# Kernel tuning notes

Measured on AMD Instinct MI355X. Metric: run time of the kernel, lower is better.

The kernel has to match this reference:

```python
import jax, jax.numpy as jnp
import numpy as np

BS, T, NOBJ = 16, 32, 100
GLOVE, GEMB, ADIM, GCN_DIM, H, ASPACE, RES = 300, 64, 10, 512, 512, 6, 512


def setup_inputs() -> dict:
    key = jax.random.key(0)
    ks = jax.random.split(key, 34)
    rn = lambda k, shp, s=0.02: (jax.random.normal(k, shp, jnp.float32) * s)
    inp = {}
    inp["target"] = jax.random.normal(ks[0], (BS, T, GLOVE), jnp.float32)
    inp["input_"] = jax.random.normal(ks[1], (BS, T, RES, 1, 1), jnp.float32)
    inp["action_probs"] = jax.random.uniform(ks[2], (BS, T, ASPACE), jnp.float32)
    # symmetric normalized adjacency (D^-1/2 A D^-1/2), as normalize_adj produces
    A_raw = (jax.random.uniform(ks[3], (NOBJ, NOBJ)) < 0.1).astype(jnp.float32)
    A_raw = ((A_raw + A_raw.T + jnp.eye(NOBJ)) > 0).astype(jnp.float32)
    dinv = 1.0 / jnp.sqrt(jnp.sum(A_raw, axis=1))
    inp["A"] = A_raw * dinv[:, None] * dinv[None, :]
    inp["all_glove"] = jax.random.normal(ks[4], (NOBJ, GLOVE), jnp.float32)
    inp["Wword"] = rn(ks[5], (GEMB, GLOVE)); inp["bword"] = jnp.zeros((GEMB,))
    inp["Wg"] = rn(ks[6], (GEMB, GLOVE)); inp["bg"] = jnp.zeros((GEMB,))
    inp["Wa"] = rn(ks[7], (ADIM, ASPACE)); inp["ba"] = jnp.zeros((ADIM,))
    inp["W0"] = rn(ks[8], (256, RES + GEMB))
    inp["W1"] = rn(ks[9], (256, 256))
    inp["W2"] = rn(ks[10], (1, 256))
    inp["Wfm"] = rn(ks[11], (GCN_DIM, NOBJ)); inp["bfm"] = jnp.zeros((GCN_DIM,))
    fused_in = RES + GEMB + ADIM + GCN_DIM
    inp["Wf"] = rn(ks[12], (H, fused_in)); inp["bf"] = jnp.zeros((H,))
    inp["Wih"] = rn(ks[13], (4 * H, H)); inp["Whh"] = rn(ks[14], (4 * H, H))
    inp["bih"] = jnp.zeros((4 * H,)); inp["bhh"] = jnp.zeros((4 * H,))
    inp["Wa1"] = rn(ks[15], (128, H)); inp["ba1"] = jnp.zeros((128,))
    inp["Wa2"] = rn(ks[16], (ASPACE, 128)); inp["ba2"] = jnp.zeros((ASPACE,))
    inp["Wc1"] = rn(ks[17], (128, H)); inp["bc1"] = jnp.zeros((128,))
    inp["Wc2"] = rn(ks[18], (1, 128)); inp["bc2"] = jnp.zeros((1,))
    return inp


def _forward(target, input_, action_probs, A, all_glove, Wword, bword, Wg, bg,
             Wa, ba, W0, W1, W2, Wfm, bfm, Wf, bf, Wih, Whh, bih, bhh,
             Wa1, ba1, Wa2, ba2, Wc1, bc1, Wc2, bc2):
    bs, t = target.shape[0], target.shape[1]
    B = bs * t
    feats = input_.reshape(B, RES)                      # [B,512] (squeeze 1x1)
    glove_e = jax.nn.relu(target.reshape(B, GLOVE) @ Wg.T + bg)
    act_e = jax.nn.relu(action_probs.reshape(B, ASPACE) @ Wa.T + ba)
    # GCN branch (all_glove is detached in the original)
    word = jax.lax.stop_gradient(all_glove) @ Wword.T + bword   # [N,GEMB]
    N = A.shape[0]
    class_e = jnp.broadcast_to(feats[:, None, :], (B, N, RES))
    x = jnp.concatenate([class_e, jnp.broadcast_to(word[None], (B, N, GEMB))], -1)
    x = jax.nn.relu(jnp.einsum('nm,bmd->bnd', A, x) @ W0.T)     # [B,N,256]
    x = jax.nn.relu(jnp.einsum('nm,bmd->bnd', A, x) @ W1.T)     # [B,N,256]
    x = jax.nn.relu(jnp.einsum('nm,bmd->bnd', A, x) @ W2.T)     # [B,N,1]
    gcn_e = x[..., 0] @ Wfm.T + bfm                             # [B,GCN_DIM]
    fused = jnp.concatenate([feats, glove_e, act_e, gcn_e], -1)
    out = jax.nn.relu(fused @ Wf.T + bf).reshape(bs, t, H)
    # LSTM (torch gate order i,f,g,o), batch_first, zero init state
    h0 = jnp.zeros((bs, H), out.dtype)
    c0 = jnp.zeros((bs, H), out.dtype)
    def step(carry, xt):
        h, c = carry
        g = xt @ Wih.T + h @ Whh.T + bih + bhh
        i, f, gg, o = jnp.split(g, 4, axis=-1)
        c = jax.nn.sigmoid(f) * c + jax.nn.sigmoid(i) * jnp.tanh(gg)
        h = jax.nn.sigmoid(o) * jnp.tanh(c)
        return (h, c), h
    (hT, cT), hs = jax.lax.scan(step, (h0, c0), out.transpose(1, 0, 2))
    sf = hs.transpose(1, 0, 2).reshape(B, H)
    actor = jax.nn.relu(jax.nn.relu(sf @ Wa1.T + ba1) @ Wa2.T + ba2).reshape(bs, t, ASPACE)
    critic = jax.nn.relu(jax.nn.relu(sf @ Wc1.T + bc1) @ Wc2.T + bc2).reshape(bs, t, 1)
    return actor, critic, hT[None], cT[None]


def reference(target, input_, action_probs, A, all_glove, Wword, bword, Wg, bg,
              Wa, ba, W0, W1, W2, Wfm, bfm, Wf, bf, Wih, Whh, bih, bhh,
              Wa1, ba1, Wa2, ba2, Wc1, bc1, Wc2, bc2):
    return _forward(target, input_, action_probs, A, all_glove, Wword, bword,
                    Wg, bg, Wa, ba, W0, W1, W2, Wfm, bfm, Wf, bf, Wih, Whh,
                    bih, bhh, Wa1, ba1, Wa2, ba2, Wc1, bc1, Wc2, bc2)
```

## Files before the change

### kernel.cpp

```cpp
#include <hip/hip_runtime.h>
#include <cmath>

constexpr int BSZ = 16, T = 32, NOBJ = 100;
constexpr int GLOVE = 300, GEMB = 64, ADIM = 10, GCN_DIM = 512, Hh = 512, ASPACE = 6, RES = 512;
constexpr int Bt = BSZ * T;
constexpr int FUSED_IN = RES + GEMB + ADIM + GCN_DIM;
constexpr int FP = 1120;

typedef __attribute__((ext_vector_type(8))) short bf16x8;
typedef __attribute__((ext_vector_type(4))) float f32x4;

__device__ __forceinline__ unsigned short f2bf(float f) {
    unsigned u = __float_as_uint(f);
    return (unsigned short)((u + 0x7FFFu + ((u >> 16) & 1u)) >> 16);
}
__device__ __forceinline__ unsigned pk2(float a, float b) {
    return (unsigned)f2bf(a) | ((unsigned)f2bf(b) << 16);
}
__device__ __forceinline__ float sigf(float x) { return 1.f / (1.f + __expf(-x)); }

template<bool RELU, int OMODE>
__global__ __launch_bounds__(256)
void mgemm(const unsigned short* __restrict__ A, int lda,
           const unsigned short* __restrict__ B, int ldb,
           float* __restrict__ Cf, unsigned short* __restrict__ Cb, int ldc,
           const float* __restrict__ bias, int K)
{
    const int tid = threadIdx.x;
    const int l = tid & 63, wv = tid >> 6;
    const int m0 = blockIdx.y * 64 + wv * 16;
    const int n0 = blockIdx.x * 64;
    const int lr = l & 15, kg = l >> 4;
    const unsigned short* ap = A + (long)(m0 + lr) * lda + kg * 8;
    const unsigned short* bp = B + (long)(n0 + lr) * ldb + kg * 8;
    const int nk = K >> 5;
    f32x4 acc0 = (f32x4){0.f, 0.f, 0.f, 0.f};
    f32x4 acc1 = acc0, acc2 = acc0, acc3 = acc0;
    bf16x8 a_[4], b0_[4], b1_[4], b2_[4], b3_[4];
#pragma unroll
    for (int s = 0; s < 4; ++s) {
        if (s < nk) {
            int k = s * 32;
            a_[s]  = *(const bf16x8*)(ap + k);
            b0_[s] = *(const bf16x8*)(bp + k);
            b1_[s] = *(const bf16x8*)(bp + 16 * ldb + k);
            b2_[s] = *(const bf16x8*)(bp + 32 * ldb + k);
            b3_[s] = *(const bf16x8*)(bp + 48 * ldb + k);
        }
    }
    for (int i = 0; i < nk; i += 4) {
#pragma unroll
        for (int s = 0; s < 4; ++s) {
            if (i + s < nk) {
                acc0 = __builtin_amdgcn_mfma_f32_16x16x32_bf16(a_[s], b0_[s], acc0, 0, 0, 0);
                acc1 = __builtin_amdgcn_mfma_f32_16x16x32_bf16(a_[s], b1_[s], acc1, 0, 0, 0);
                acc2 = __builtin_amdgcn_mfma_f32_16x16x32_bf16(a_[s], b2_[s], acc2, 0, 0, 0);
                acc3 = __builtin_amdgcn_mfma_f32_16x16x32_bf16(a_[s], b3_[s], acc3, 0, 0, 0);
                if (i + s + 4 < nk) {
                    int k = (i + s + 4) * 32;
                    a_[s]  = *(const bf16x8*)(ap + k);
                    b0_[s] = *(const bf16x8*)(bp + k);
                    b1_[s] = *(const bf16x8*)(bp + 16 * ldb + k);
                    b2_[s] = *(const bf16x8*)(bp + 32 * ldb + k);
                    b3_[s] = *(const bf16x8*)(bp + 48 * ldb + k);
                }
            }
        }
    }
    f32x4 av[4] = {acc0, acc1, acc2, acc3};
#pragma unroll
    for (int nf = 0; nf < 4; ++nf) {
        int n = n0 + nf * 16 + lr;
        float bs = bias ? bias[n] : 0.f;
#pragma unroll
        for (int r = 0; r < 4; ++r) {
            float val = av[nf][r] + bs;
            if (RELU) val = fmaxf(val, 0.f);
            long idx = (long)(m0 + kg * 4 + r) * ldc + n;
            if (OMODE == 0) Cf[idx] = val;
            else            Cb[idx] = f2bf(val);
        }
    }
}

template<bool RELU>
__global__ __launch_bounds__(128)
void gemm32(const float* __restrict__ A, int lda,
            const float* __restrict__ B, int ldb,
            float* __restrict__ C, int ldc,
            const float* __restrict__ bias, int M, int N, int K)
{
    __shared__ float As[32][36];
    __shared__ float Bs[32][68];
    const int tid = threadIdx.x;
    const int m0 = blockIdx.y * 32, n0 = blockIdx.x * 64;
    const int mi = tid >> 4, ni = tid & 15;
    float acc[4][4] = {};
    for (int k0 = 0; k0 < K; k0 += 32) {
        __syncthreads();
#pragma unroll
        for (int l = 0; l < 2; ++l) {
            int e = tid + l * 128;
            int row = e >> 3, kq = (e & 7) << 2;
            float4 va = make_float4(0.f, 0.f, 0.f, 0.f);
            if (m0 + row < M && k0 + kq < K)
                va = *(const float4*)&A[(long)(m0 + row) * lda + k0 + kq];
            As[kq + 0][row] = va.x; As[kq + 1][row] = va.y;
            As[kq + 2][row] = va.z; As[kq + 3][row] = va.w;
        }
#pragma unroll
        for (int l = 0; l < 4; ++l) {
            int e = tid + l * 128;
            int row = e >> 3, kq = (e & 7) << 2;
            float4 vb = make_float4(0.f, 0.f, 0.f, 0.f);
            if (n0 + row < N && k0 + kq < K)
                vb = *(const float4*)&B[(long)(n0 + row) * ldb + k0 + kq];
            Bs[kq + 0][row] = vb.x; Bs[kq + 1][row] = vb.y;
            Bs[kq + 2][row] = vb.z; Bs[kq + 3][row] = vb.w;
        }
        __syncthreads();
#pragma unroll
        for (int k = 0; k < 32; ++k) {
            float4 a4 = *(const float4*)&As[k][4 * mi];
            float4 b4 = *(const float4*)&Bs[k][4 * ni];
            acc[0][0] = fmaf(a4.x, b4.x, acc[0][0]); acc[0][1] = fmaf(a4.x, b4.y, acc[0][1]);
            acc[0][2] = fmaf(a4.x, b4.z, acc[0][2]); acc[0][3] = fmaf(a4.x, b4.w, acc[0][3]);
            acc[1][0] = fmaf(a4.y, b4.x, acc[1][0]); acc[1][1] = fmaf(a4.y, b4.y, acc[1][1]);
            acc[1][2] = fmaf(a4.y, b4.z, acc[1][2]); acc[1][3] = fmaf(a4.y, b4.w, acc[1][3]);
            acc[2][0] = fmaf(a4.z, b4.x, acc[2][0]); acc[2][1] = fmaf(a4.z, b4.y, acc[2][1]);
            acc[2][2] = fmaf(a4.z, b4.z, acc[2][2]); acc[2][3] = fmaf(a4.z, b4.w, acc[2][3]);
            acc[3][0] = fmaf(a4.w, b4.x, acc[3][0]); acc[3][1] = fmaf(a4.w, b4.y, acc[3][1]);
            acc[3][2] = fmaf(a4.w, b4.z, acc[3][2]); acc[3][3] = fmaf(a4.w, b4.w, acc[3][3]);
        }
    }
    const int n = n0 + 4 * ni;
    if (n >= N) return;
    float4 bv = make_float4(0.f, 0.f, 0.f, 0.f);
    if (bias) bv = *(const float4*)&bias[n];
#pragma unroll
    for (int r = 0; r < 4; ++r) {
        int m = m0 + 4 * mi + r;
        if (m >= M) continue;
        float4 v;
        v.x = acc[r][0] + bv.x; v.y = acc[r][1] + bv.y;
        v.z = acc[r][2] + bv.z; v.w = acc[r][3] + bv.w;
        if (RELU) {
            v.x = fmaxf(v.x, 0.f); v.y = fmaxf(v.y, 0.f);
            v.z = fmaxf(v.z, 0.f); v.w = fmaxf(v.w, 0.f);
        }
        *(float4*)&C[(long)m * ldc + n] = v;
    }
}

__global__ __launch_bounds__(256)
void x1pack(const float* __restrict__ u, const float* __restrict__ v,
            const float* __restrict__ rowsum, uint4* __restrict__ X1g)
{
    __shared__ float u_lds[256];
    __shared__ float rs_lds[112];
    const int b = blockIdx.x, tid = threadIdx.x;
    u_lds[tid] = u[(long)b * 256 + tid];
    if (tid < 112) rs_lds[tid] = (tid < 100) ? rowsum[tid] : 0.f;
    __syncthreads();
    uint4* outp = X1g + (size_t)b * 3584;
#pragma unroll
    for (int it = 0; it < 14; ++it) {
        int job = it * 256 + tid;
        int l = job & 63;
        int kt = (job >> 6) & 7;
        int mt = job >> 9;
        int n = mt * 16 + (l & 15);
        int k0 = kt * 32 + ((l >> 4) << 3);
        uint4 p = make_uint4(0, 0, 0, 0);
        if (n < 100) {
            float rsn = rs_lds[n];
            float4 u0 = *(const float4*)&u_lds[k0];
            float4 u1 = *(const float4*)&u_lds[k0 + 4];
            const float4* vp = (const float4*)&v[n * 256 + k0];
            float4 v0 = vp[0], v1 = vp[1];
            float x0 = fmaxf(fmaf(rsn, u0.x, v0.x), 0.f), x1 = fmaxf(fmaf(rsn, u0.y, v0.y), 0.f);
            float x2 = fmaxf(fmaf(rsn, u0.z, v0.z), 0.f), x3 = fmaxf(fmaf(rsn, u0.w, v0.w), 0.f);
            float x4 = fmaxf(fmaf(rsn, u1.x, v1.x), 0.f), x5 = fmaxf(fmaf(rsn, u1.y, v1.y), 0.f);
            float x6 = fmaxf(fmaf(rsn, u1.z, v1.z), 0.f), x7 = fmaxf(fmaf(rsn, u1.w, v1.w), 0.f);
            p = make_uint4(pk2(x0, x1), pk2(x2, x3), pk2(x4, x5), pk2(x6, x7));
        }
        outp[job] = p;
    }
}

constexpr int ZLD = 152;

__global__ __launch_bounds__(256, 2)
void gcn_core(const bf16x8* __restrict__ X1g,
              const float* __restrict__ Aglob,
              const bf16x8* __restrict__ W1f,
              const bf16x8* __restrict__ Af,
              const float* __restrict__ w2,
              unsigned short* __restrict__ x3b)
{
    __shared__ unsigned short Z1Ts[128 * ZLD];
    __shared__ float w2l[256];
    __shared__ float spart[4][112];
    __shared__ float sl[112];

    const int b = blockIdx.x, tid = threadIdx.x;
    const int l = tid & 63, wv = tid >> 6;
    const int lrow = l & 15, kg = l >> 4;

    w2l[tid] = w2[tid];
    if (tid < 128) {
        uint4 z = make_uint4(0, 0, 0, 0);
        *(uint4*)&Z1Ts[tid * ZLD + 112] = z;
        *(uint4*)&Z1Ts[tid * ZLD + 120] = z;
    }
    if (tid < 28) x3b[(long)b * 128 + 100 + tid] = 0;
    __syncthreads();

    const bf16x8* xb = X1g + (size_t)b * 3584 + l;

    float sacc[7][4];
#pragma unroll
    for (int mt = 0; mt < 7; ++mt)
#pragma unroll
        for (int r = 0; r < 4; ++r) sacc[mt][r] = 0.f;

    for (int half = 0; half < 2; ++half) {
        f32x4 acc1[7][2];
#pragma unroll
        for (int mt = 0; mt < 7; ++mt)
#pragma unroll
            for (int jtl = 0; jtl < 2; ++jtl) acc1[mt][jtl] = (f32x4){0.f, 0.f, 0.f, 0.f};

#pragma unroll
        for (int kt = 0; kt < 8; ++kt) {
            bf16x8 af[7];
#pragma unroll
            for (int mt = 0; mt < 7; ++mt)
                af[mt] = xb[mt * 512 + kt * 64];
#pragma unroll
            for (int jtl = 0; jtl < 2; ++jtl) {
                int jt = half * 8 + wv * 2 + jtl;
                bf16x8 bfr = W1f[(jt * 8 + kt) * 64 + l];
#pragma unroll
                for (int mt = 0; mt < 7; ++mt)
                    acc1[mt][jtl] = __builtin_amdgcn_mfma_f32_16x16x32_bf16(af[mt], bfr, acc1[mt][jtl], 0, 0, 0);
            }
        }

#pragma unroll
        for (int mt = 0; mt < 7; ++mt)
#pragma unroll
            for (int jtl = 0; jtl < 2; ++jtl) {
                int jloc = (wv * 2 + jtl) * 16 + lrow;
                f32x4 a = acc1[mt][jtl];
                uint2 zz;
                zz.x = pk2(a[0], a[1]);
                zz.y = pk2(a[2], a[3]);
                *(uint2*)&Z1Ts[jloc * ZLD + mt * 16 + kg * 4] = zz;
            }

        bf16x8 bz[2][4];
#pragma unroll
        for (int jtl = 0; jtl < 2; ++jtl)
#pragma unroll
            for (int k2 = 0; k2 < 4; ++k2)
                bz[jtl][k2] = *(const bf16x8*)&Z1Ts[((wv * 2 + jtl) * 16 + lrow) * ZLD + k2 * 32 + kg * 8];
#pragma unroll
        for (int mt = 0; mt < 7; ++mt) {
            bf16x8 aA[4];
#pragma unroll
            for (int k2 = 0; k2 < 4; ++k2) aA[k2] = Af[(mt * 4 + k2) * 64 + l];
#pragma unroll
            for (int jtl = 0; jtl < 2; ++jtl) {
                f32x4 p = (f32x4){0.f, 0.f, 0.f, 0.f};
#pragma unroll
                for (int k2 = 0; k2 < 4; ++k2)
                    p = __builtin_amdgcn_mfma_f32_16x16x32_bf16(aA[k2], bz[jtl][k2], p, 0, 0, 0);
                float w2j = w2l[half * 128 + (wv * 2 + jtl) * 16 + lrow];
#pragma unroll
                for (int r = 0; r < 4; ++r)
                    sacc[mt][r] = fmaf(fmaxf(p[r], 0.f), w2j, sacc[mt][r]);
            }
        }
    }

#pragma unroll
    for (int mt = 0; mt < 7; ++mt) {
        float s0 = sacc[mt][0], s1 = sacc[mt][1], s2 = sacc[mt][2], s3 = sacc[mt][3];
#pragma unroll
        for (int off = 1; off < 16; off <<= 1) {
            s0 += __shfl_xor(s0, off);
            s1 += __shfl_xor(s1, off);
            s2 += __shfl_xor(s2, off);
            s3 += __shfl_xor(s3, off);
        }
        if (lrow == 0) {
            int m = mt * 16 + kg * 4;
            spart[wv][m + 0] = s0; spart[wv][m + 1] = s1;
            spart[wv][m + 2] = s2; spart[wv][m + 3] = s3;
        }
    }
    __syncthreads();
    if (tid < 112)
        sl[tid] = spart[0][tid] + spart[1][tid] + spart[2][tid] + spart[3][tid];
    __syncthreads();

    float sv0 = (l < 100) ? sl[l] : 0.f;
    float sv1 = (l + 64 < 100) ? sl[l + 64] : 0.f;
#pragma unroll 5
    for (int i = 0; i < 25; ++i) {
        int n = i * 4 + wv;
        float a0 = (l < 100) ? Aglob[n * 100 + l] : 0.f;
        float a1 = (l + 64 < 100) ? Aglob[n * 100 + l + 64] : 0.f;
        float p = a0 * sv0 + a1 * sv1;
#pragma unroll
        for (int off = 32; off; off >>= 1) p += __shfl_xor(p, off);
        if (l == 0) x3b[(long)b * 128 + n] = f2bf(fmaxf(p, 0.f));
    }
}

__global__ __launch_bounds__(256)
void lstm_persist(const float* __restrict__ xWih,
                  const bf16x8* __restrict__ Whhf,
                  unsigned short* __restrict__ hbA,
                  unsigned short* __restrict__ hbB,
                  float* __restrict__ cBuf,
                  float* __restrict__ hFin,
                  unsigned short* __restrict__ sfb,
                  unsigned* __restrict__ bar)
{
    __shared__ float gl[4][16][17];
    const int tid = threadIdx.x;
    const int l = tid & 63, g = tid >> 6;
    const int bid = blockIdx.x;
    const int jt = g * 32 + bid;
    const int lr = l & 15, kg = l >> 4;
    const bf16x8* wp = Whhf + (size_t)jt * 16 * 64 + l;
    bf16x8 w[16];
#pragma unroll
    for (int kt = 0; kt < 16; ++kt) w[kt] = wp[kt * 64];
    const int fb = tid >> 4, jl = tid & 15;
    const int jh = bid * 16 + jl;
    float c_reg = 0.f;
    const unsigned short* hprev = hbA;
    unsigned short* hnext = hbB;
    for (int t = 0; t < T; ++t) {
        const unsigned short* hp = hprev + lr * 512 + kg * 8;
        f32x4 acc = (f32x4){0.f, 0.f, 0.f, 0.f};
#pragma unroll
        for (int kt = 0; kt < 16; ++kt) {
            bf16x8 a = *(const bf16x8*)(hp + kt * 32);
            acc = __builtin_amdgcn_mfma_f32_16x16x32_bf16(a, w[kt], acc, 0, 0, 0);
        }
#pragma unroll
        for (int r = 0; r < 4; ++r) gl[g][kg * 4 + r][lr] = acc[r];
        __syncthreads();
        const float* xw = xWih + (size_t)(fb * T + t) * 2048;
        float gi = gl[0][fb][jl] + xw[jh];
        float gf = gl[1][fb][jl] + xw[512 + jh];
        float gg = gl[2][fb][jl] + xw[1024 + jh];
        float go = gl[3][fb][jl] + xw[1536 + jh];
        float cn = sigf(gf) * c_reg + sigf(gi) * tanhf(gg);
        float hn = sigf(go) * tanhf(cn);
        c_reg = cn;
        hnext[fb * 512 + jh] = f2bf(hn);
        sfb[(size_t)(fb * T + t) * 512 + jh] = f2bf(hn);
        if (t == T - 1) { hFin[fb * 512 + jh] = hn; cBuf[fb * 512 + jh] = cn; }
        __syncthreads();
        if (tid == 0) {
            __threadfence();
            atomicAdd(bar, 1u);
            unsigned target = 32u * (unsigned)(t + 1);
            while (atomicAdd(bar, 0u) < target) { }
            __threadfence();
        }
        __syncthreads();
        const unsigned short* tmp = hprev; hprev = hnext; hnext = (unsigned short*)tmp;
    }
}

__global__ void k_aw_rowsum(const float* __restrict__ A, const float* __restrict__ word,
                            float* __restrict__ Aw, float* __restrict__ rowsum)
{
    int i = blockIdx.x * 256 + threadIdx.x;
    if (i < 6400) {
        int n = i / 64, k = i % 64;
        float s = 0.f;
        for (int m = 0; m < 100; ++m) s += A[n * 100 + m] * word[m * 64 + k];
        Aw[i] = s;
    } else if (i < 6500) {
        int n = i - 6400;
        float s = 0.f;
        for (int m = 0; m < 100; ++m) s += A[n * 100 + m];
        rowsum[n] = s;
    }
}

__global__ void k_prep(const float* __restrict__ Whh, uint4* __restrict__ Whhf,
                       const float* __restrict__ Wf, unsigned short* __restrict__ WfPb,
                       const float* __restrict__ Wih, unsigned short* __restrict__ Wihb,
                       const float* __restrict__ Wa1, const float* __restrict__ Wc1,
                       unsigned short* __restrict__ Whdb,
                       const float* __restrict__ ba1, const float* __restrict__ bc1,
                       float* __restrict__ bhd,
                       const float* __restrict__ Wg, unsigned short* __restrict__ Wgb,
                       const float* __restrict__ W0, unsigned short* __restrict__ W0ab,
                       const float* __restrict__ Wfm, unsigned short* __restrict__ Wfmb,
                       const float* __restrict__ target, unsigned short* __restrict__ tgtb,
                       const float* __restrict__ feats, unsigned short* __restrict__ featsb,
                       unsigned short* __restrict__ fusedb,
                       const float* __restrict__ aprob, const float* __restrict__ Wa,
                       const float* __restrict__ ba,
                       unsigned short* __restrict__ hbA, unsigned* __restrict__ bar,
                       const float* __restrict__ bih, const float* __restrict__ bhh,
                       float* __restrict__ bsum,
                       const float* __restrict__ W1, uint4* __restrict__ W1f,
                       const float* __restrict__ A, uint4* __restrict__ Af)
{
    int bx = blockIdx.x, tid = threadIdx.x;
    if (bx < 512) {
        int job = bx * 256 + tid;
        int jtkt = job >> 6, ll = job & 63;
        int j = (jtkt >> 4) * 16 + (ll & 15);
        int k0 = (jtkt & 15) * 32 + (ll >> 4) * 8;
        const float* src = &Whh[(long)j * 512 + k0];
        uint4 p;
        p.x = pk2(src[0], src[1]); p.y = pk2(src[2], src[3]);
        p.z = pk2(src[4], src[5]); p.w = pk2(src[6], src[7]);
        Whhf[job] = p;
    } else if (bx < 2752) {
        int i = (bx - 512) * 256 + tid;
        int r = i / FP, c = i - r * FP;
        WfPb[i] = f2bf(c < FUSED_IN ? Wf[(long)r * FUSED_IN + c] : 0.f);
    } else if (bx < 6848) {
        int i = (bx - 2752) * 256 + tid;
        Wihb[i] = f2bf(Wih[i]);
    } else if (bx < 7360) {
        int i = (bx - 6848) * 256 + tid;
        int r = i >> 9, c = i & 511;
        Whdb[i] = f2bf(r < 128 ? Wa1[r * 512 + c] : Wc1[(r - 128) * 512 + c]);
    } else if (bx < 7361) {
        bhd[tid] = (tid < 128) ? ba1[tid] : bc1[tid - 128];
    } else if (bx < 7441) {
        int i = (bx - 7361) * 256 + tid;
        int r = i / 320, c = i - r * 320;
        Wgb[i] = f2bf(c < GLOVE ? Wg[r * GLOVE + c] : 0.f);
    } else if (bx < 7953) {
        int i = (bx - 7441) * 256 + tid;
        int r = i >> 9, c = i & 511;
        W0ab[i] = f2bf(W0[(long)r * 576 + c]);
    } else if (bx < 8209) {
        int i = (bx - 7953) * 256 + tid;
        int r = i >> 7, c = i & 127;
        Wfmb[i] = f2bf(c < 100 ? Wfm[r * 100 + c] : 0.f);
    } else if (bx < 8849) {
        int i = (bx - 8209) * 256 + tid;
        int r = i / 320, c = i - r * 320;
        tgtb[i] = f2bf(c < GLOVE ? target[(long)r * GLOVE + c] : 0.f);
    } else if (bx < 9873) {
        int i = (bx - 8849) * 256 + tid;
        featsb[i] = f2bf(feats[i]);
    } else if (bx < 10897) {
        int i = (bx - 9873) * 256 + tid;
        int r = i >> 9, c = i & 511;
        fusedb[(long)r * FP + c] = f2bf(feats[i]);
    } else if (bx < 10917) {
        int i = (bx - 10897) * 256 + tid;
        int r = i / 10, c6 = i - r * 10;
        float s = ba[c6];
#pragma unroll
        for (int k = 0; k < 6; ++k) s += aprob[r * 6 + k] * Wa[c6 * 6 + k];
        fusedb[(long)r * FP + 576 + c6] = f2bf(fmaxf(s, 0.f));
    } else if (bx < 10961) {
        int i = (bx - 10917) * 256 + tid;
        int r = i / 22, c = 1098 + (i - r * 22);
        fusedb[(long)r * FP + c] = 0;
    } else if (bx < 10993) {
        int i = (bx - 10961) * 256 + tid;
        hbA[i] = 0;
    } else if (bx < 10994) {
        if (tid == 0) bar[0] = 0u;
    } else if (bx < 11002) {
        int i = (bx - 10994) * 256 + tid;
        bsum[i] = bih[i] + bhh[i];
    } else if (bx < 11034) {
        int job = (bx - 11002) * 256 + tid;
        int jt = job >> 9, rem = job & 511, kt = rem >> 6, lane = rem & 63;
        int j = jt * 16 + (lane & 15), k0 = kt * 32 + (lane >> 4) * 8;
        const float* src = &W1[(long)j * 256 + k0];
        uint4 p;
        p.x = pk2(src[0], src[1]); p.y = pk2(src[2], src[3]);
        p.z = pk2(src[4], src[5]); p.w = pk2(src[6], src[7]);
        W1f[job] = p;
    } else {
        int job = (bx - 11034) * 256 + tid;
        int mt = job >> 8, rem = job & 255, kt = rem >> 6, lane = rem & 63;
        int m = mt * 16 + (lane & 15), n0 = kt * 32 + (lane >> 4) * 8;
        float h[8];
#pragma unroll
        for (int e = 0; e < 8; ++e)
            h[e] = (m < 100 && n0 + e < 100) ? A[m * 100 + n0 + e] : 0.f;
        uint4 p;
        p.x = pk2(h[0], h[1]); p.y = pk2(h[2], h[3]);
        p.z = pk2(h[4], h[5]); p.w = pk2(h[6], h[7]);
        Af[job] = p;
    }
}

__global__ void k_finish(const float* __restrict__ hd,
                         const float* __restrict__ Wa2, const float* __restrict__ ba2,
                         const float* __restrict__ Wc2, const float* __restrict__ bc2,
                         const float* __restrict__ hFin, const float* __restrict__ cBuf,
                         float* __restrict__ out)
{
    if (blockIdx.x < 32) {
        int row = blockIdx.x * 16 + (threadIdx.x >> 4);
        int slot = threadIdx.x & 15;
        if (slot < 6) {
            const float4* h4 = (const float4*)(hd + (long)row * 256);
            const float4* w4 = (const float4*)(Wa2 + slot * 128);
            float s = 0.f;
#pragma unroll
            for (int k = 0; k < 32; ++k) {
                float4 h = h4[k], w = w4[k];
                s += h.x * w.x + h.y * w.y + h.z * w.z + h.w * w.w;
            }
            out[row * 6 + slot] = fmaxf(s + ba2[slot], 0.f);
        } else if (slot == 6) {
            const float4* h4 = (const float4*)(hd + (long)row * 256 + 128);
            const float4* w4 = (const float4*)(Wc2);
            float s = 0.f;
#pragma unroll
            for (int k = 0; k < 32; ++k) {
                float4 h = h4[k], w = w4[k];
                s += h.x * w.x + h.y * w.y + h.z * w.z + h.w * w.w;
            }
            out[3072 + row] = fmaxf(s + bc2[0], 0.f);
        }
    } else {
        int i = (blockIdx.x - 32) * 256 + threadIdx.x;
        out[3584 + i] = hFin[i];
        out[11776 + i] = cBuf[i];
    }
}

static inline void mg(hipStream_t st, const unsigned short* A, int lda,
                      const unsigned short* B, int ldb,
                      float* Cf, unsigned short* Cb, int ldc,
                      const float* bias, int M, int N, int K, bool relu, bool bf16out)
{
    dim3 g(N / 64, M / 64), blk(256);
    if (bf16out) {
        if (relu) hipLaunchKernelGGL((mgemm<true, 1>), g, blk, 0, st, A, lda, B, ldb, Cf, Cb, ldc, bias, K);
        else      hipLaunchKernelGGL((mgemm<false, 1>), g, blk, 0, st, A, lda, B, ldb, Cf, Cb, ldc, bias, K);
    } else {
        if (relu) hipLaunchKernelGGL((mgemm<true, 0>), g, blk, 0, st, A, lda, B, ldb, Cf, Cb, ldc, bias, K);
        else      hipLaunchKernelGGL((mgemm<false, 0>), g, blk, 0, st, A, lda, B, ldb, Cf, Cb, ldc, bias, K);
    }
}
static inline void g32(hipStream_t st, const float* A, int lda, const float* B, int ldb,
                       float* C, int ldc, const float* bias, int M, int N, int K, bool relu)
{
    dim3 g((N + 63) / 64, (M + 31) / 32), blk(128);
    if (relu) hipLaunchKernelGGL((gemm32<true>), g, blk, 0, st, A, lda, B, ldb, C, ldc, bias, M, N, K);
    else      hipLaunchKernelGGL((gemm32<false>), g, blk, 0, st, A, lda, B, ldb, C, ldc, bias, M, N, K);
}

extern "C" void kernel_launch(void* const* d_in, const int* in_sizes, int n_in,
                              void* d_out, int out_size, void* d_ws, size_t ws_size,
                              hipStream_t stream)
{
    const float* target = (const float*)d_in[0];
    const float* input_ = (const float*)d_in[1];
    const float* aprob  = (const float*)d_in[2];
    const float* Adj    = (const float*)d_in[3];
    const float* aglove = (const float*)d_in[4];
    const float* Wword  = (const float*)d_in[5];
    const float* bword  = (const float*)d_in[6];
    const float* Wg     = (const float*)d_in[7];
    const float* bg     = (const float*)d_in[8];
    const float* Wa     = (const float*)d_in[9];
    const float* ba     = (const float*)d_in[10];
    const float* W0     = (const float*)d_in[11];
    const float* W1     = (const float*)d_in[12];
    const float* W2     = (const float*)d_in[13];
    const float* Wfm    = (const float*)d_in[14];
    const float* bfm    = (const float*)d_in[15];
    const float* Wf     = (const float*)d_in[16];
    const float* bf     = (const float*)d_in[17];
    const float* Wih    = (const float*)d_in[18];
    const float* Whh    = (const float*)d_in[19];
    const float* bih    = (const float*)d_in[20];
    const float* bhh    = (const float*)d_in[21];
    const float* Wa1    = (const float*)d_in[22];
    const float* ba1    = (const float*)d_in[23];
    const float* Wa2    = (const float*)d_in[24];
    const float* ba2    = (const float*)d_in[25];
    const float* Wc1    = (const float*)d_in[26];
    const float* bc1    = (const float*)d_in[27];
    const float* Wc2    = (const float*)d_in[28];
    const float* bc2    = (const float*)d_in[29];

    float* ws = (float*)d_ws;
    float* out = (float*)d_out;

    size_t off = 0;
    auto alloc = [&](size_t n) { size_t r = off; off += (n + 255) & ~(size_t)255; return r; };
    float* u       = ws + alloc(512 * 256);
    float* word    = ws + alloc(100 * 64);
    float* Aw      = ws + alloc(100 * 64);
    float* rowsum  = ws + alloc(128);
    float* v       = ws + alloc(100 * 256);
    float* bsum    = ws + alloc(2048);
    float* bhd     = ws + alloc(256);
    float* xWih    = ws + alloc((size_t)512 * 2048);
    float* hd      = ws + alloc(512 * 256);
    float* hFin    = ws + alloc(BSZ * Hh);
    float* cBuf    = ws + alloc(BSZ * Hh);
    float* W1frag  = ws + alloc(32768);
    float* Afrag   = ws + alloc(7168);
    float* Whhf    = ws + alloc((size_t)524288);
    float* X1gf    = ws + alloc((size_t)512 * 3584 * 4);
    unsigned* bar  = (unsigned*)(ws + alloc(256));
    unsigned short* x3b     = (unsigned short*)(ws + alloc(512 * 128 / 2));
    unsigned short* fusedb  = (unsigned short*)(ws + alloc((size_t)512 * FP / 2));
    unsigned short* WfPb    = (unsigned short*)(ws + alloc((size_t)512 * FP / 2));
    unsigned short* outfb   = (unsigned short*)(ws + alloc(512 * 512 / 2));
    unsigned short* Wihb    = (unsigned short*)(ws + alloc((size_t)2048 * 512 / 2));
    unsigned short* Whdb    = (unsigned short*)(ws + alloc(256 * 512 / 2));
    unsigned short* Wgb     = (unsigned short*)(ws + alloc(64 * 320 / 2));
    unsigned short* W0ab    = (unsigned short*)(ws + alloc(256 * 512 / 2));
    unsigned short* Wfmb    = (unsigned short*)(ws + alloc(512 * 128 / 2));
    unsigned short* tgtb    = (unsigned short*)(ws + alloc(512 * 320 / 2));
    unsigned short* featsb  = (unsigned short*)(ws + alloc(512 * 512 / 2));
    unsigned short* sfb     = (unsigned short*)(ws + alloc(512 * 512 / 2));
    unsigned short* hbA     = (unsigned short*)(ws + alloc(BSZ * Hh / 2));
    unsigned short* hbB     = (unsigned short*)(ws + alloc(BSZ * Hh / 2));
    (void)ws_size; (void)in_sizes; (void)n_in; (void)out_size;

    const float* feats = input_;

    hipLaunchKernelGGL(k_prep, dim3(11041), dim3(256), 0, stream,
                       Whh, (uint4*)Whhf, Wf, WfPb, Wih, Wihb, Wa1, Wc1, Whdb, ba1, bc1, bhd,
                       Wg, Wgb, W0, W0ab, Wfm, Wfmb, target, tgtb, feats, featsb,
                       fusedb, aprob, Wa, ba, hbA, bar, bih, bhh, bsum,
                       W1, (uint4*)W1frag, Adj, (uint4*)Afrag);

    g32(stream, aglove, GLOVE, Wword, GLOVE, word, 64, bword, 100, 64, GLOVE, false);
    hipLaunchKernelGGL(k_aw_rowsum, dim3(26), dim3(256), 0, stream, Adj, word, Aw, rowsum);
    g32(stream, Aw, 64, W0 + 512, 576, v, 256, nullptr, 100, 256, 64, false);

    mg(stream, featsb, 512, W0ab, 512, u, nullptr, 256, nullptr, 512, 256, 512, false, false);
    mg(stream, tgtb, 320, Wgb, 320, nullptr, fusedb + 512, FP, bg, 512, 64, 320, true, true);

    hipLaunchKernelGGL(x1pack, dim3(Bt), dim3(256), 0, stream, u, v, rowsum, (uint4*)X1gf);
    hipLaunchKernelGGL(gcn_core, dim3(Bt), dim3(256), 0, stream,
                       (const bf16x8*)X1gf, Adj, (const bf16x8*)W1frag, (const bf16x8*)Afrag, W2, x3b);
    mg(stream, x3b, 128, Wfmb, 128, nullptr, fusedb + 586, FP, bfm, 512, 512, 128, false, true);

    mg(stream, fusedb, FP, WfPb, FP, nullptr, outfb, 512, bf, 512, 512, FP, true, true);
    mg(stream, outfb, 512, Wihb, 512, xWih, nullptr, 2048, bsum, 512, 2048, 512, false, false);

    hipLaunchKernelGGL(lstm_persist, dim3(32), dim3(256), 0, stream,
                       xWih, (const bf16x8*)Whhf, hbA, hbB, cBuf, hFin, sfb, bar);

    mg(stream, sfb, 512, Whdb, 512, hd, nullptr, 256, bhd, 512, 256, 512, true, false);
    hipLaunchKernelGGL(k_finish, dim3(64), dim3(256), 0, stream,
                       hd, Wa2, ba2, Wc2, bc2, hFin, cBuf, out);
}
```

Measured before the change: 380.5 us.

## Use relaxed agent-scope atomics and staged 64-bit stores in persistent LSTM barrier

Rewrites the persistent LSTM's grid barrier and hidden-state exchange. The full-fence atomics and the tight spin loop become relaxed agent-scope atomics with s_sleep backoff. Hidden-state tiles are staged in shared memory and published with 64-bit atomic stores, and the next step reads them with atomic loads. This is meant to cut fence and coherence cost on each of the 32 sequential steps. Dropping the explicit fences relies on relaxed atomics plus workgroup barriers giving enough ordering, which may be fragile.

```diff
diff --git a/kernel.cpp b/kernel.cpp
--- a/kernel.cpp
+++ b/kernel.cpp
@@ -319,17 +319,19 @@
     }
 }
 
+union HU { unsigned long long u[2]; bf16x8 v; };
+
 __global__ __launch_bounds__(256)
-void lstm_persist(const float* __restrict__ xWih,
-                  const bf16x8* __restrict__ Whhf,
-                  unsigned short* __restrict__ hbA,
-                  unsigned short* __restrict__ hbB,
-                  float* __restrict__ cBuf,
-                  float* __restrict__ hFin,
-                  unsigned short* __restrict__ sfb,
-                  unsigned* __restrict__ bar)
+void lstm_persist2(const float* __restrict__ xWih,
+                   const bf16x8* __restrict__ Whhf,
+                   unsigned long long* __restrict__ h0,
+                   unsigned long long* __restrict__ h1,
+                   float* __restrict__ cBuf, float* __restrict__ hFin,
+                   unsigned short* __restrict__ sfb,
+                   unsigned* __restrict__ bar)
 {
     __shared__ float gl[4][16][17];
+    __shared__ unsigned short htile[16][16];
     const int tid = threadIdx.x;
     const int l = tid & 63, g = tid >> 6;
     const int bid = blockIdx.x;
@@ -342,16 +344,20 @@
     const int fb = tid >> 4, jl = tid & 15;
     const int jh = bid * 16 + jl;
     float c_reg = 0.f;
-    const unsigned short* hprev = hbA;
-    unsigned short* hnext = hbB;
+    unsigned long long* hprev = h0;
+    unsigned long long* hnext = h1;
     for (int t = 0; t < T; ++t) {
-        const unsigned short* hp = hprev + lr * 512 + kg * 8;
+        const unsigned long long* hp = hprev + lr * 128 + kg * 2;
+        HU hu[16];
+#pragma unroll
+        for (int kt = 0; kt < 16; ++kt) {
+            hu[kt].u[0] = __hip_atomic_load(hp + kt * 8,     __ATOMIC_RELAXED, __HIP_MEMORY_SCOPE_AGENT);
+            hu[kt].u[1] = __hip_atomic_load(hp + kt * 8 + 1, __ATOMIC_RELAXED, __HIP_MEMORY_SCOPE_AGENT);
+        }
         f32x4 acc = (f32x4){0.f, 0.f, 0.f, 0.f};
 #pragma unroll
-        for (int kt = 0; kt < 16; ++kt) {
-            bf16x8 a = *(const bf16x8*)(hp + kt * 32);
-            acc = __builtin_amdgcn_mfma_f32_16x16x32_bf16(a, w[kt], acc, 0, 0, 0);
-        }
+        for (int kt = 0; kt < 16; ++kt)
+            acc = __builtin_amdgcn_mfma_f32_16x16x32_bf16(hu[kt].v, w[kt], acc, 0, 0, 0);
 #pragma unroll
         for (int r = 0; r < 4; ++r) gl[g][kg * 4 + r][lr] = acc[r];
         __syncthreads();
@@ -363,19 +369,26 @@
         float cn = sigf(gf) * c_reg + sigf(gi) * tanhf(gg);
         float hn = sigf(go) * tanhf(cn);
         c_reg = cn;
-        hnext[fb * 512 + jh] = f2bf(hn);
-        sfb[(size_t)(fb * T + t) * 512 + jh] = f2bf(hn);
+        unsigned short hb = f2bf(hn);
+        htile[fb][jl] = hb;
+        sfb[(size_t)(fb * T + t) * 512 + jh] = hb;
         if (t == T - 1) { hFin[fb * 512 + jh] = hn; cBuf[fb * 512 + jh] = cn; }
         __syncthreads();
+        if (tid < 64) {
+            int row = tid >> 2, q = tid & 3;
+            unsigned long long val = *(const unsigned long long*)&htile[row][q * 4];
+            __hip_atomic_store(&hnext[row * 128 + bid * 4 + q], val,
+                               __ATOMIC_RELAXED, __HIP_MEMORY_SCOPE_AGENT);
+        }
+        __syncthreads();
         if (tid == 0) {
-            __threadfence();
-            atomicAdd(bar, 1u);
-            unsigned target = 32u * (unsigned)(t + 1);
-            while (atomicAdd(bar, 0u) < target) { }
-            __threadfence();
+            __hip_atomic_fetch_add(bar, 1u, __ATOMIC_RELAXED, __HIP_MEMORY_SCOPE_AGENT);
+            unsigned tgt = 32u * (unsigned)(t + 1);
+            while (__hip_atomic_load(bar, __ATOMIC_RELAXED, __HIP_MEMORY_SCOPE_AGENT) < tgt)
+                __builtin_amdgcn_s_sleep(1);
         }
         __syncthreads();
-        const unsigned short* tmp = hprev; hprev = hnext; hnext = (unsigned short*)tmp;
+        unsigned long long* tmp = hprev; hprev = hnext; hnext = tmp;
     }
 }
 
@@ -661,8 +674,10 @@
     mg(stream, fusedb, FP, WfPb, FP, nullptr, outfb, 512, bf, 512, 512, FP, true, true);
     mg(stream, outfb, 512, Wihb, 512, xWih, nullptr, 2048, bsum, 512, 2048, 512, false, false);
 
-    hipLaunchKernelGGL(lstm_persist, dim3(32), dim3(256), 0, stream,
-                       xWih, (const bf16x8*)Whhf, hbA, hbB, cBuf, hFin, sfb, bar);
+    hipLaunchKernelGGL(lstm_persist2, dim3(32), dim3(256), 0, stream,
+                       xWih, (const bf16x8*)Whhf,
+                       (unsigned long long*)hbA, (unsigned long long*)hbB,
+                       cBuf, hFin, sfb, bar);
 
     mg(stream, sfb, 512, Whdb, 512, hd, nullptr, 256, bhd, 512, 256, 512, true, false);
     hipLaunchKernelGGL(k_finish, dim3(64), dim3(256), 0, stream,
```

Measured after the change: 375.5 us. No clear change (-1.3%).
